# Optimization experiments

Measured on AMD Instinct MI355X. Metric: run time of the kernel, lower is better.

## Reference

```python
import jax, jax.numpy as jnp
import numpy as np

B, T, E, H, D = 4, 2048, 1024, 16, 64  # batch, seq(block_size), n_embed, num_heads, hidden_dim


def setup_inputs() -> dict:
    key = jax.random.key(0)
    ks = jax.random.split(key, 10)
    s_in = 1.0 / np.sqrt(E)
    return {
        "x": jax.random.normal(ks[0], (B, T, E), dtype=jnp.float32),
        "Wq": jax.random.normal(ks[1], (H, E, D), dtype=jnp.float32) * s_in,
        "bq": jnp.zeros((H, D), dtype=jnp.float32),
        "Wk": jax.random.normal(ks[2], (H, E, D), dtype=jnp.float32) * s_in,
        "bk": jnp.zeros((H, D), dtype=jnp.float32),
        "Wv": jax.random.normal(ks[3], (H, E, D), dtype=jnp.float32) * s_in,
        "bv": jnp.zeros((H, D), dtype=jnp.float32),
        "Wp": jax.random.normal(ks[4], (E, E), dtype=jnp.float32) * s_in,
        "bp": jnp.zeros((E,), dtype=jnp.float32),
    }


def reference(x, Wq, bq, Wk, bk, Wv, bv, Wp, bp):
    # Batched equivalent of the per-head Python loop: each head h computes
    # causal scaled-dot-product attention with its own Q/K/V projections.
    q = jnp.einsum("bte,hed->bhtd", x, Wq) + bq[None, :, None, :]
    k = jnp.einsum("bte,hed->bhtd", x, Wk) + bk[None, :, None, :]
    v = jnp.einsum("bte,hed->bhtd", x, Wv) + bv[None, :, None, :]
    scale = 1.0 / jnp.sqrt(jnp.asarray(D, dtype=x.dtype))
    scores = jnp.einsum("bhtd,bhsd->bhts", q, k) * scale  # [B,H,T,T]
    causal = jnp.tril(jnp.ones((T, T), dtype=bool))
    scores = jnp.where(causal[None, None, :, :], scores, jnp.asarray(-jnp.inf, dtype=x.dtype))
    att = jax.nn.softmax(scores, axis=-1)
    head_out = jnp.einsum("bhts,bhsd->bhtd", att, v)  # [B,H,T,D]
    # concat heads along last dim: [B,T,H*D] == [B,T,E]
    cat = head_out.transpose(0, 2, 1, 3).reshape(B, T, H * D)
    out = cat @ Wp + bp  # final projection (dropout is identity in eval)
    return out
```

## Files before the change

### kernel.cpp

```cpp
#include <hip/hip_runtime.h>


typedef __attribute__((ext_vector_type(8))) __bf16 bf16x8;
typedef __attribute__((ext_vector_type(4))) float f32x4;
typedef __attribute__((ext_vector_type(16))) float f32x16;
typedef __attribute__((ext_vector_type(4))) unsigned int u32x4;
typedef __attribute__((ext_vector_type(2))) unsigned int u32x2;
typedef unsigned short u16;
typedef unsigned int u32;

#define DEV __device__ __forceinline__

#define QK_SCALE 0.18033688011112042f

DEV u16 f2bf(float f) {
  u32 u = __builtin_bit_cast(u32, f);
  u += 0x7fffu + ((u >> 16) & 1u);
  return (u16)(u >> 16);
}
DEV u32 pack2(float a, float b) { return (u32)f2bf(a) | ((u32)f2bf(b) << 16); }

DEV float exp2_hw(float x) { float r; asm("v_exp_f32 %0, %1" : "=v"(r) : "v"(x)); return r; }
DEV u32 cvtpk_bf16(float lo, float hi) {
  u32 r; asm("v_cvt_pk_bf16_f32 %0, %1, %2" : "=v"(r) : "v"(lo), "v"(hi)); return r;
}
DEV void pl32swap(u32& a, u32& b) { asm("v_permlane32_swap_b32 %0, %1" : "+v"(a), "+v"(b)); }

DEV f32x16 zero16() { f32x16 z;
#pragma unroll
  for (int i = 0; i < 16; i++) z[i] = 0.f;
  return z; }

__global__ __launch_bounds__(256) void prep_x_kernel(
    const float* __restrict__ x, const float* __restrict__ bq, const float* __restrict__ bk,
    const float* __restrict__ bv, u16* __restrict__ xbf, float* __restrict__ bqkv) {
  int gid = blockIdx.x * 256 + threadIdx.x;
  if (gid < 3072) {
    float v = (gid < 1024) ? bq[gid] * QK_SCALE : (gid < 2048 ? bk[gid - 1024] : bv[gid - 2048]);
    bqkv[gid] = v;
  }
  const float4* xv = (const float4*)x;
  float4 f0 = xv[(size_t)gid * 2];
  float4 f1 = xv[(size_t)gid * 2 + 1];
  u32x4 st;
  st.x = pack2(f0.x, f0.y); st.y = pack2(f0.z, f0.w);
  st.z = pack2(f1.x, f1.y); st.w = pack2(f1.z, f1.w);
  *(u32x4*)&xbf[(size_t)gid * 8] = st;
}

__global__ __launch_bounds__(256) void prep_w_kernel(
    const float* __restrict__ Wq, const float* __restrict__ Wk, const float* __restrict__ Wv,
    const float* __restrict__ Wp, u16* __restrict__ wqkvT, u16* __restrict__ wpT) {
  __shared__ float t[64][65];
  int bid = blockIdx.x, tid = threadIdx.x;
  int r0 = tid >> 6, c = tid & 63;
  if (bid < 768) {
    int p = bid >> 8, rem = bid & 255, h = rem >> 4, et = rem & 15;
    float sc = (p == 0) ? QK_SCALE : 1.0f;
    const float* src = (p == 0 ? Wq : (p == 1 ? Wk : Wv)) + ((size_t)h * 1024 + et * 64) * 64;
#pragma unroll
    for (int i = 0; i < 16; i++) { int e = r0 + i * 4; t[e][c] = src[(size_t)e * 64 + c]; }
    __syncthreads();
    u16* dst = wqkvT + ((size_t)p * 1024 + h * 64) * 1024 + et * 64;
#pragma unroll
    for (int i = 0; i < 16; i++) { int d = r0 + i * 4; dst[(size_t)d * 1024 + c] = f2bf(t[c][d] * sc); }
  } else {
    int b2 = bid - 768, rt = b2 >> 4, ct = b2 & 15;
#pragma unroll
    for (int i = 0; i < 16; i++) { int e = r0 + i * 4; t[e][c] = Wp[(size_t)(rt * 64 + e) * 1024 + ct * 64 + c]; }
    __syncthreads();
#pragma unroll
    for (int i = 0; i < 16; i++) { int f = r0 + i * 4; wpT[(size_t)(ct * 64 + f) * 1024 + rt * 64 + c] = f2bf(t[c][f]); }
  }
}

DEV void stage_tile(const u16* __restrict__ X, int row0, int k0, u16* lds, int tid) {
#pragma unroll
  for (int j = 0; j < 4; j++) {
    int ci = j * 256 + tid;
    int row = ci >> 3, slot = ci & 7;
    int srcslot = slot ^ (row & 7);
    const u16* gp = X + (size_t)(row0 + row) * 1024 + k0 + srcslot * 8;
    __builtin_amdgcn_global_load_lds((const __attribute__((address_space(1))) void*)gp,
                                     (__attribute__((address_space(3))) void*)(lds + ci * 8),
                                     16, 0, 0);
  }
}

__global__ __launch_bounds__(256) void gemm128_kernel(
    const u16* __restrict__ A, const u16* __restrict__ Bt, const float* __restrict__ bias,
    int tilesN, int mode, u16* __restrict__ Qb, u16* __restrict__ Kb, u16* __restrict__ VTb,
    float* __restrict__ outF) {
  __shared__ u16 As[128 * 64];
  __shared__ u16 Bs[128 * 64];
  int nwg = gridDim.x;
  int bid = blockIdx.x;
  int swz = (bid % 8) * (nwg / 8) + bid / 8;
  int bm = swz / tilesN, bn = swz % tilesN;
  int tid = threadIdx.x;
  int lane = tid & 63, wave = tid >> 6;
  int wm = wave >> 1, wn = wave & 1;
  int lr = lane & 15, lg = lane >> 4;

  f32x4 acc[4][4];
#pragma unroll
  for (int i = 0; i < 4; i++)
#pragma unroll
    for (int j = 0; j < 4; j++) acc[i][j] = f32x4{0.f, 0.f, 0.f, 0.f};

  for (int k0 = 0; k0 < 1024; k0 += 64) {
    stage_tile(A, bm * 128, k0, As, tid);
    stage_tile(Bt, bn * 128, k0, Bs, tid);
    __syncthreads();
#pragma unroll
    for (int kf = 0; kf < 2; kf++) {
      bf16x8 af[4], bfr[4];
#pragma unroll
      for (int i = 0; i < 4; i++) {
        int ra = wm * 64 + i * 16 + lr;
        af[i] = *(const bf16x8*)&As[ra * 64 + (((lg + kf * 4) ^ (ra & 7)) * 8)];
        int rb = wn * 64 + i * 16 + lr;
        bfr[i] = *(const bf16x8*)&Bs[rb * 64 + (((lg + kf * 4) ^ (rb & 7)) * 8)];
      }
      __builtin_amdgcn_s_setprio(1);
#pragma unroll
      for (int i = 0; i < 4; i++)
#pragma unroll
        for (int j = 0; j < 4; j++)
          acc[i][j] = __builtin_amdgcn_mfma_f32_16x16x32_bf16(af[i], bfr[j], acc[i][j], 0, 0, 0);
      __builtin_amdgcn_s_setprio(0);
    }
    __syncthreads();
  }

  int crow = bm * 128 + wm * 64;
  int ccol = bn * 128 + wn * 64;
  if (mode == 0) {
#pragma unroll
    for (int j = 0; j < 4; j++) {
      int col = ccol + j * 16 + lr;
      float bb = bias[col];
      int p = col >> 10, h = (col >> 6) & 15, d = col & 63;
#pragma unroll
      for (int i = 0; i < 4; i++) {
        int row0 = crow + i * 16 + lg * 4;
        int b_ = row0 >> 11, t0 = row0 & 2047;
        if (p == 2) {
          u32x2 pv;
          pv.x = pack2(acc[i][j][0] + bb, acc[i][j][1] + bb);
          pv.y = pack2(acc[i][j][2] + bb, acc[i][j][3] + bb);
          *(u32x2*)&VTb[((size_t)(b_ * 16 + h) * 64 + d) * 2048 + t0] = pv;
        } else {
          u16* dst = (p == 0 ? Qb : Kb);
#pragma unroll
          for (int r = 0; r < 4; r++)
            dst[((size_t)(b_ * 16 + h) * 2048 + (t0 + r)) * 64 + d] = f2bf(acc[i][j][r] + bb);
        }
      }
    }
  } else {
#pragma unroll
    for (int j = 0; j < 4; j++) {
      int col = ccol + j * 16 + lr;
      float bb = bias[col];
#pragma unroll
      for (int i = 0; i < 4; i++) {
        int row0 = crow + i * 16 + lg * 4;
#pragma unroll
        for (int r = 0; r < 4; r++)
          outF[(size_t)(row0 + r) * 1024 + col] = acc[i][j][r] + bb;
      }
    }
  }
}

DEV void stage_kv(const u16* __restrict__ Kh, const u16* __restrict__ Vh, int kv0,
                  u16* Ksb, u16* Vsb, int tid) {
#pragma unroll
  for (int j = 0; j < 2; j++) {
    int ci = j * 256 + tid;
    int row = ci >> 3, slot = ci & 7;
    int ss = slot ^ (row & 7);
    __builtin_amdgcn_global_load_lds(
        (const __attribute__((address_space(1))) void*)(Kh + (size_t)(kv0 + row) * 64 + ss * 8),
        (__attribute__((address_space(3))) void*)(Ksb + ci * 8), 16, 0, 0);
    __builtin_amdgcn_global_load_lds(
        (const __attribute__((address_space(1))) void*)(Vh + (size_t)row * 2048 + kv0 + ss * 8),
        (__attribute__((address_space(3))) void*)(Vsb + ci * 8), 16, 0, 0);
  }
}

__global__ __launch_bounds__(256, 4) void attn_kernel(
    const u16* __restrict__ Qb, const u16* __restrict__ Kb, const u16* __restrict__ VTb,
    u16* __restrict__ cat) {
  __shared__ u16 Ks[2][64 * 64];
  __shared__ u16 Vs[2][64 * 64];
  int bid = blockIdx.x;
  int t = bid >> 6;
  int bh = bid & 63;
  int b = bh >> 4, h = bh & 15;
  int tid = threadIdx.x, wave = tid >> 6, lane = tid & 63;
  int l31 = lane & 31, hi = lane >> 5;
  int qrow = (l31 < 16) ? (t * 64 + wave * 16 + l31)
                        : ((31 - t) * 64 + wave * 16 + (l31 - 16));

  const u16* Qh = Qb + (size_t)bh * 2048 * 64;
  const u16* Kh = Kb + (size_t)bh * 2048 * 64;
  const u16* Vh = VTb + (size_t)bh * 64 * 2048;

  bf16x8 qf[4];
#pragma unroll
  for (int ks = 0; ks < 4; ks++)
    qf[ks] = *(const bf16x8*)&Qh[(size_t)qrow * 64 + ks * 16 + hi * 8];

  f32x16 o0 = zero16(), o1 = zero16();
  float m_run = -1e30f, l_run = 0.f;
  int iters = 32 - t;

  stage_kv(Kh, Vh, 0, Ks[0], Vs[0], tid);
  __syncthreads();
  int cur = 0;

  for (int kvt = 0; kvt < iters; ++kvt) {
    int kv0 = kvt * 64;
    if (kvt + 1 < iters) stage_kv(Kh, Vh, kv0 + 64, Ks[cur ^ 1], Vs[cur ^ 1], tid);

    f32x16 s0 = zero16(), s1 = zero16();
    __builtin_amdgcn_s_setprio(1);
#pragma unroll
    for (int ks = 0; ks < 4; ks++) {
      int r0 = l31, r1 = 32 + l31;
      bf16x8 k0 = *(const bf16x8*)&Ks[cur][r0 * 64 + (((ks * 2 + hi) ^ (r0 & 7)) * 8)];
      bf16x8 k1 = *(const bf16x8*)&Ks[cur][r1 * 64 + (((ks * 2 + hi) ^ (r1 & 7)) * 8)];
      s0 = __builtin_amdgcn_mfma_f32_32x32x16_bf16(k0, qf[ks], s0, 0, 0, 0);
      s1 = __builtin_amdgcn_mfma_f32_32x32x16_bf16(k1, qf[ks], s1, 0, 0, 0);
    }
    __builtin_amdgcn_s_setprio(0);

    if (__any(kv0 + 63 > qrow)) {
      int relh = qrow - kv0 - 4 * hi;
#pragma unroll
      for (int r = 0; r < 16; r++) {
        int off = (r & 3) + 8 * (r >> 2);
        s0[r] = (off > relh) ? -1e30f : s0[r];
        s1[r] = (off + 32 > relh) ? -1e30f : s1[r];
      }
    }

    float tm0 = fmaxf(s0[0], s1[0]), tm1 = fmaxf(s0[1], s1[1]);
    float tm2 = fmaxf(s0[2], s1[2]), tm3 = fmaxf(s0[3], s1[3]);
#pragma unroll
    for (int j = 1; j < 4; j++) {
      tm0 = fmaxf(tm0, fmaxf(s0[j * 4 + 0], s1[j * 4 + 0]));
      tm1 = fmaxf(tm1, fmaxf(s0[j * 4 + 1], s1[j * 4 + 1]));
      tm2 = fmaxf(tm2, fmaxf(s0[j * 4 + 2], s1[j * 4 + 2]));
      tm3 = fmaxf(tm3, fmaxf(s0[j * 4 + 3], s1[j * 4 + 3]));
    }
    float tmax = fmaxf(fmaxf(tm0, tm1), fmaxf(tm2, tm3));
    tmax = fmaxf(tmax, __shfl_xor(tmax, 32));
    float corr = 1.f;
    if (!__all(tmax <= m_run + 8.f)) {
      float m_new = fmaxf(m_run, tmax);
      corr = exp2_hw(m_run - m_new);
      o0 = o0 * corr;
      o1 = o1 * corr;
      m_run = m_new;
    }
    float t0 = 0.f, t1 = 0.f, t2 = 0.f, t3 = 0.f;
#pragma unroll
    for (int j = 0; j < 4; j++) {
      float p00 = exp2_hw(s0[j * 4 + 0] - m_run); s0[j * 4 + 0] = p00; t0 += p00;
      float p01 = exp2_hw(s0[j * 4 + 1] - m_run); s0[j * 4 + 1] = p01; t1 += p01;
      float p02 = exp2_hw(s0[j * 4 + 2] - m_run); s0[j * 4 + 2] = p02; t2 += p02;
      float p03 = exp2_hw(s0[j * 4 + 3] - m_run); s0[j * 4 + 3] = p03; t3 += p03;
      float p10 = exp2_hw(s1[j * 4 + 0] - m_run); s1[j * 4 + 0] = p10; t0 += p10;
      float p11 = exp2_hw(s1[j * 4 + 1] - m_run); s1[j * 4 + 1] = p11; t1 += p11;
      float p12 = exp2_hw(s1[j * 4 + 2] - m_run); s1[j * 4 + 2] = p12; t2 += p12;
      float p13 = exp2_hw(s1[j * 4 + 3] - m_run); s1[j * 4 + 3] = p13; t3 += p13;
    }
    float ts = (t0 + t1) + (t2 + t3);
    ts += __shfl_xor(ts, 32);
    l_run = l_run * corr + ts;

    __builtin_amdgcn_s_setprio(1);
#pragma unroll
    for (int ks = 0; ks < 4; ks++) {
      const f32x16& sb = (ks < 2) ? s0 : s1;
      int g2 = (ks & 1) * 8;
      u32 a  = cvtpk_bf16(sb[g2 + 0], sb[g2 + 1]);
      u32 c  = cvtpk_bf16(sb[g2 + 2], sb[g2 + 3]);
      u32 bb = cvtpk_bf16(sb[g2 + 4], sb[g2 + 5]);
      u32 d  = cvtpk_bf16(sb[g2 + 6], sb[g2 + 7]);
      pl32swap(a, bb);
      pl32swap(c, d);
      u32x4 wv; wv.x = a; wv.y = c; wv.z = bb; wv.w = d;
      bf16x8 pf = __builtin_bit_cast(bf16x8, wv);
      int r0 = l31, r1 = 32 + l31;
      bf16x8 v0 = *(const bf16x8*)&Vs[cur][r0 * 64 + (((ks * 2 + hi) ^ (r0 & 7)) * 8)];
      bf16x8 v1 = *(const bf16x8*)&Vs[cur][r1 * 64 + (((ks * 2 + hi) ^ (r1 & 7)) * 8)];
      o0 = __builtin_amdgcn_mfma_f32_32x32x16_bf16(v0, pf, o0, 0, 0, 0);
      o1 = __builtin_amdgcn_mfma_f32_32x32x16_bf16(v1, pf, o1, 0, 0, 0);
    }
    __builtin_amdgcn_s_setprio(0);

    __syncthreads();
    cur ^= 1;
  }

  float li = 1.0f / l_run;
#pragma unroll
  for (int m = 0; m < 8; m++) {
    int dbase = 2 * (m & 1) + 8 * (m >> 1) + 4 * hi;
    u32 w0 = cvtpk_bf16(o0[2 * m] * li, o0[2 * m + 1] * li);
    u32 w1 = cvtpk_bf16(o1[2 * m] * li, o1[2 * m + 1] * li);
    *(u32*)&cat[(size_t)(b * 2048 + qrow) * 1024 + h * 64 + dbase] = w0;
    *(u32*)&cat[(size_t)(b * 2048 + qrow) * 1024 + h * 64 + 32 + dbase] = w1;
  }
}

extern "C" void kernel_launch(void* const* d_in, const int* in_sizes, int n_in,
                              void* d_out, int out_size, void* d_ws, size_t ws_size,
                              hipStream_t stream) {
  const float* x  = (const float*)d_in[0];
  const float* Wq = (const float*)d_in[1];
  const float* bq = (const float*)d_in[2];
  const float* Wk = (const float*)d_in[3];
  const float* bk = (const float*)d_in[4];
  const float* Wv = (const float*)d_in[5];
  const float* bv = (const float*)d_in[6];
  const float* Wp = (const float*)d_in[7];
  const float* bp = (const float*)d_in[8];

  char* w = (char*)d_ws;
  u16* xbf    = (u16*)w;                 w += (size_t)8192 * 1024 * 2;
  u16* wqkvT  = (u16*)w;                 w += (size_t)3072 * 1024 * 2;
  u16* wpT    = (u16*)w;                 w += (size_t)1024 * 1024 * 2;
  float* bqkv = (float*)w;               w += (size_t)3072 * 4;
  u16* Qb     = (u16*)w;                 w += (size_t)64 * 2048 * 64 * 2;
  u16* Kb     = (u16*)w;                 w += (size_t)64 * 2048 * 64 * 2;
  u16* VTb    = (u16*)w;                 w += (size_t)64 * 64 * 2048 * 2;
  u16* cat    = (u16*)w;                 w += (size_t)8192 * 1024 * 2;

  prep_x_kernel<<<4096, 256, 0, stream>>>(x, bq, bk, bv, xbf, bqkv);
  prep_w_kernel<<<1024, 256, 0, stream>>>(Wq, Wk, Wv, Wp, wqkvT, wpT);
  gemm128_kernel<<<1536, 256, 0, stream>>>(xbf, wqkvT, bqkv, 24, 0, Qb, Kb, VTb, nullptr);
  attn_kernel<<<1024, 256, 0, stream>>>(Qb, Kb, VTb, cat);
  gemm128_kernel<<<512, 256, 0, stream>>>(cat, wpT, bp, 8, 1, nullptr, nullptr, nullptr, (float*)d_out);
}
```

Baseline: 181.8 us.

## Give each attention block one causal query tile and schedule heavy tiles first

Before, each 256-thread block paired query rows from tile t with rows from tile 31-t, so both halves of every wave iterated over the longer KV range. Rows from the short tile spent most of those iterations on fully masked work. Now each 128-thread block owns a single 64-row tile, with each wave handling 32 contiguous rows, and runs exactly t+1 KV iterations. Masking is applied only on the diagonal tile. Blocks are ordered longest-first to reduce tail imbalance. The change also precomputes LDS swizzle offsets and uses v_max3 for the row max. The trade-off is smaller blocks with a different launch bound, which changes occupancy and per-block staging cost.

```diff
diff --git a/kernel.cpp b/kernel.cpp
--- a/kernel.cpp
+++ b/kernel.cpp
@@ -25,6 +25,9 @@
   u32 r; asm("v_cvt_pk_bf16_f32 %0, %1, %2" : "=v"(r) : "v"(lo), "v"(hi)); return r;
 }
 DEV void pl32swap(u32& a, u32& b) { asm("v_permlane32_swap_b32 %0, %1" : "+v"(a), "+v"(b)); }
+DEV float max3f(float a, float b, float c) {
+  float r; asm("v_max3_f32 %0, %1, %2, %3" : "=v"(r) : "v"(a), "v"(b), "v"(c)); return r;
+}
 
 DEV f32x16 zero16() { f32x16 z;
 #pragma unroll
@@ -174,11 +177,11 @@
   }
 }
 
-DEV void stage_kv(const u16* __restrict__ Kh, const u16* __restrict__ Vh, int kv0,
-                  u16* Ksb, u16* Vsb, int tid) {
-#pragma unroll
-  for (int j = 0; j < 2; j++) {
-    int ci = j * 256 + tid;
+DEV void stage_kv128(const u16* __restrict__ Kh, const u16* __restrict__ Vh, int kv0,
+                     u16* Ksb, u16* Vsb, int tid) {
+#pragma unroll
+  for (int j = 0; j < 4; j++) {
+    int ci = j * 128 + tid;
     int row = ci >> 3, slot = ci & 7;
     int ss = slot ^ (row & 7);
     __builtin_amdgcn_global_load_lds(
@@ -190,19 +193,18 @@
   }
 }
 
-__global__ __launch_bounds__(256, 4) void attn_kernel(
+__global__ __launch_bounds__(128, 2) void attn_kernel(
     const u16* __restrict__ Qb, const u16* __restrict__ Kb, const u16* __restrict__ VTb,
     u16* __restrict__ cat) {
   __shared__ u16 Ks[2][64 * 64];
   __shared__ u16 Vs[2][64 * 64];
   int bid = blockIdx.x;
-  int t = bid >> 6;
+  int t = 31 - (bid >> 6);
   int bh = bid & 63;
   int b = bh >> 4, h = bh & 15;
   int tid = threadIdx.x, wave = tid >> 6, lane = tid & 63;
   int l31 = lane & 31, hi = lane >> 5;
-  int qrow = (l31 < 16) ? (t * 64 + wave * 16 + l31)
-                        : ((31 - t) * 64 + wave * 16 + (l31 - 16));
+  int qrow = t * 64 + wave * 32 + l31;
 
   const u16* Qh = Qb + (size_t)bh * 2048 * 64;
   const u16* Kh = Kb + (size_t)bh * 2048 * 64;
@@ -213,31 +215,36 @@
   for (int ks = 0; ks < 4; ks++)
     qf[ks] = *(const bf16x8*)&Qh[(size_t)qrow * 64 + ks * 16 + hi * 8];
 
+  u32 loff[4];
+#pragma unroll
+  for (int ks = 0; ks < 4; ks++)
+    loff[ks] = (u32)(l31 * 128 + (((ks * 2 + hi) ^ (l31 & 7)) * 16));
+
   f32x16 o0 = zero16(), o1 = zero16();
   float m_run = -1e30f, l_run = 0.f;
-  int iters = 32 - t;
-
-  stage_kv(Kh, Vh, 0, Ks[0], Vs[0], tid);
+  int iters = t + 1;
+
+  stage_kv128(Kh, Vh, 0, Ks[0], Vs[0], tid);
   __syncthreads();
   int cur = 0;
 
   for (int kvt = 0; kvt < iters; ++kvt) {
     int kv0 = kvt * 64;
-    if (kvt + 1 < iters) stage_kv(Kh, Vh, kv0 + 64, Ks[cur ^ 1], Vs[cur ^ 1], tid);
+    if (kvt + 1 < iters) stage_kv128(Kh, Vh, kv0 + 64, Ks[cur ^ 1], Vs[cur ^ 1], tid);
 
     f32x16 s0 = zero16(), s1 = zero16();
+    const char* kb = (const char*)&Ks[cur][0];
     __builtin_amdgcn_s_setprio(1);
 #pragma unroll
     for (int ks = 0; ks < 4; ks++) {
-      int r0 = l31, r1 = 32 + l31;
-      bf16x8 k0 = *(const bf16x8*)&Ks[cur][r0 * 64 + (((ks * 2 + hi) ^ (r0 & 7)) * 8)];
-      bf16x8 k1 = *(const bf16x8*)&Ks[cur][r1 * 64 + (((ks * 2 + hi) ^ (r1 & 7)) * 8)];
+      bf16x8 k0 = *(const bf16x8*)(kb + loff[ks]);
+      bf16x8 k1 = *(const bf16x8*)(kb + loff[ks] + 4096);
       s0 = __builtin_amdgcn_mfma_f32_32x32x16_bf16(k0, qf[ks], s0, 0, 0, 0);
       s1 = __builtin_amdgcn_mfma_f32_32x32x16_bf16(k1, qf[ks], s1, 0, 0, 0);
     }
     __builtin_amdgcn_s_setprio(0);
 
-    if (__any(kv0 + 63 > qrow)) {
+    if (kvt == t) {
       int relh = qrow - kv0 - 4 * hi;
 #pragma unroll
       for (int r = 0; r < 16; r++) {
@@ -247,16 +254,22 @@
       }
     }
 
-    float tm0 = fmaxf(s0[0], s1[0]), tm1 = fmaxf(s0[1], s1[1]);
-    float tm2 = fmaxf(s0[2], s1[2]), tm3 = fmaxf(s0[3], s1[3]);
-#pragma unroll
-    for (int j = 1; j < 4; j++) {
-      tm0 = fmaxf(tm0, fmaxf(s0[j * 4 + 0], s1[j * 4 + 0]));
-      tm1 = fmaxf(tm1, fmaxf(s0[j * 4 + 1], s1[j * 4 + 1]));
-      tm2 = fmaxf(tm2, fmaxf(s0[j * 4 + 2], s1[j * 4 + 2]));
-      tm3 = fmaxf(tm3, fmaxf(s0[j * 4 + 3], s1[j * 4 + 3]));
-    }
-    float tmax = fmaxf(fmaxf(tm0, tm1), fmaxf(tm2, tm3));
+    float ta = max3f(s0[0], s0[1], s0[2]);
+    float tb = max3f(s0[4], s0[5], s0[6]);
+    float tc = max3f(s0[8], s0[9], s0[10]);
+    float td = max3f(s0[12], s0[13], s0[14]);
+    ta = max3f(ta, s0[3], s1[0]);
+    tb = max3f(tb, s0[7], s1[4]);
+    tc = max3f(tc, s0[11], s1[8]);
+    td = max3f(td, s0[15], s1[12]);
+    ta = max3f(ta, s1[1], s1[2]);
+    tb = max3f(tb, s1[5], s1[6]);
+    tc = max3f(tc, s1[9], s1[10]);
+    td = max3f(td, s1[13], s1[14]);
+    ta = max3f(ta, s1[3], tb);
+    tc = max3f(tc, s1[7], td);
+    float tmax = max3f(ta, tc, s1[11]);
+    tmax = fmaxf(tmax, s1[15]);
     tmax = fmaxf(tmax, __shfl_xor(tmax, 32));
     float corr = 1.f;
     if (!__all(tmax <= m_run + 8.f)) {
@@ -282,6 +295,7 @@
     ts += __shfl_xor(ts, 32);
     l_run = l_run * corr + ts;
 
+    const char* vb = (const char*)&Vs[cur][0];
     __builtin_amdgcn_s_setprio(1);
 #pragma unroll
     for (int ks = 0; ks < 4; ks++) {
@@ -295,9 +309,8 @@
       pl32swap(c, d);
       u32x4 wv; wv.x = a; wv.y = c; wv.z = bb; wv.w = d;
       bf16x8 pf = __builtin_bit_cast(bf16x8, wv);
-      int r0 = l31, r1 = 32 + l31;
-      bf16x8 v0 = *(const bf16x8*)&Vs[cur][r0 * 64 + (((ks * 2 + hi) ^ (r0 & 7)) * 8)];
-      bf16x8 v1 = *(const bf16x8*)&Vs[cur][r1 * 64 + (((ks * 2 + hi) ^ (r1 & 7)) * 8)];
+      bf16x8 v0 = *(const bf16x8*)(vb + loff[ks]);
+      bf16x8 v1 = *(const bf16x8*)(vb + loff[ks] + 4096);
       o0 = __builtin_amdgcn_mfma_f32_32x32x16_bf16(v0, pf, o0, 0, 0, 0);
       o1 = __builtin_amdgcn_mfma_f32_32x32x16_bf16(v1, pf, o1, 0, 0, 0);
     }
@@ -344,6 +357,6 @@
   prep_x_kernel<<<4096, 256, 0, stream>>>(x, bq, bk, bv, xbf, bqkv);
   prep_w_kernel<<<1024, 256, 0, stream>>>(Wq, Wk, Wv, Wp, wqkvT, wpT);
   gemm128_kernel<<<1536, 256, 0, stream>>>(xbf, wqkvT, bqkv, 24, 0, Qb, Kb, VTb, nullptr);
-  attn_kernel<<<1024, 256, 0, stream>>>(Qb, Kb, VTb, cat);
+  attn_kernel<<<2048, 128, 0, stream>>>(Qb, Kb, VTb, cat);
   gemm128_kernel<<<512, 256, 0, stream>>>(cat, wpT, bp, 8, 1, nullptr, nullptr, nullptr, (float*)d_out);
 }
```

Result: faster. 167.4 us (-7.9%).
